# Optimization experiments

Measured on AMD Instinct MI355X. Metric: run time of the kernel, lower is better.

The kernel has to match this reference:

```python
import jax, jax.numpy as jnp
import numpy as np

B = 16384      # batch (rollout size)
OBS = 64       # obs_dim
ACT = 8        # action_dim
H = 128        # hidden_dim
NN = 4         # num_neighbors
N = NN + 1     # num_nodes in local graph
HEADS = 2
SLOPE = 0.2    # leaky_relu negative slope


def setup_inputs() -> dict:
    key = jax.random.key(0)
    ks = jax.random.split(key, 20)

    def glorot(k, shape):
        fan_in, fan_out = shape[0], shape[-1]
        lim = np.sqrt(6.0 / (fan_in + fan_out)).astype(np.float32)
        return jax.random.uniform(k, shape, jnp.float32, -lim, lim)

    obs = jax.random.normal(ks[0], (B, OBS), jnp.float32)
    neighbor_obs = jax.random.normal(ks[1], (B, NN, OBS), jnp.float32)
    adj = jax.random.randint(ks[2], (B, N), 0, 2, jnp.int32)
    adj = adj.at[:, 0].set(1)  # self node always connected (avoids all -inf rows)

    params = dict(
        enc_w1=glorot(ks[3], (OBS, H)), enc_b1=jnp.zeros((H,), jnp.float32),
        enc_w2=glorot(ks[4], (H, H)),  enc_b2=jnp.zeros((H,), jnp.float32),
        gat_w=glorot(ks[5], (HEADS, H, H)),       # per-head W (no bias)
        gat_a=glorot(ks[6], (HEADS, 2 * H)),      # per-head attention vector a
        val_w1=glorot(ks[7], (H * HEADS, H)), val_b1=jnp.zeros((H,), jnp.float32),
        val_w2=glorot(ks[8], (H, 1)),          val_b2=jnp.zeros((1,), jnp.float32),
        pol_w1=glorot(ks[9], (H * HEADS, H)), pol_b1=jnp.zeros((H,), jnp.float32),
        pol_w2=glorot(ks[10], (H, ACT)),       pol_b2=jnp.zeros((ACT,), jnp.float32),
    )
    return {"obs": obs, "neighbor_obs": neighbor_obs, "adj": adj, **params}


def reference(obs, neighbor_obs, adj,
              enc_w1, enc_b1, enc_w2, enc_b2,
              gat_w, gat_a,
              val_w1, val_b1, val_w2, val_b2,
              pol_w1, pol_b1, pol_w2, pol_b2):
    # shared local encoder applied to self obs and each neighbor obs
    all_obs = jnp.concatenate([obs[:, None, :], neighbor_obs], axis=1)   # [B,N,OBS]
    emb = jax.nn.relu(all_obs @ enc_w1 + enc_b1) @ enc_w2 + enc_b2       # [B,N,H]

    # GAT layer (all heads vectorized). Concat attention a^T[Wh_i||Wh_j]
    # decomposes into a1.Wh_i + a2.Wh_j.
    Wh = jnp.einsum('bnd,hdo->bhno', emb, gat_w)                          # [B,heads,N,H]
    a1, a2 = gat_a[:, :H], gat_a[:, H:]
    ei = jnp.einsum('bhno,ho->bhn', Wh, a1)                               # [B,heads,N]
    ej = jnp.einsum('bhno,ho->bhn', Wh, a2)
    e = jax.nn.leaky_relu(ei[..., :, None] + ej[..., None, :], SLOPE)     # [B,heads,N,N]
    # torch masked_fill broadcasts adj [B,N] as a column mask over j
    e = jnp.where((adj == 0)[:, None, None, :], -jnp.inf, e)
    attn = jax.nn.softmax(e, axis=-1)                                     # [B,heads,N,N]
    h_prime = jnp.einsum('bhij,bhjo->bhio', attn, Wh)                     # [B,heads,N,H]

    # node 0 (the agent itself), heads concatenated (head-major order, as torch cat)
    final = h_prime[:, :, 0, :].reshape(h_prime.shape[0], HEADS * H)      # [B,heads*H]

    value = jax.nn.relu(final @ val_w1 + val_b1) @ val_w2 + val_b2        # [B,1]
    logits = jax.nn.relu(final @ pol_w1 + pol_b1) @ pol_w2 + pol_b2      # [B,ACT]
    return value, logits
```

## Files before the change

kernel.cpp:

```cpp
#include <hip/hip_runtime.h>
#include <hip/hip_bf16.h>

#define B_TOT 16384

typedef __attribute__((ext_vector_type(8))) short short8;
typedef __attribute__((ext_vector_type(4))) short short4v;
typedef __attribute__((ext_vector_type(4))) float f32x4;

__device__ __forceinline__ float bf2f(short s){
  unsigned u = ((unsigned)(unsigned short)s) << 16;
  return __uint_as_float(u);
}
__device__ __forceinline__ short f2bf(float f){
  __hip_bfloat16 h = __float2bfloat16(f);
  return *reinterpret_cast<short*>(&h);
}

#define MFMA16(a,b,c) __builtin_amdgcn_mfma_f32_16x16x32_bf16(a,b,c,0,0,0)

#define W_W1T   0
#define W_W2T   8192
#define W_GWT   24576
#define W_HW1T  57344
#define W_PW2T  122880
#define W_VW2   123904
#define W_NELEM 124032
#define CVEC_BYTE 248064
#define MIX_BYTE  250112
#define PREP_TOT  124544

__global__ void prep_weights(const float* __restrict__ enc_w1, const float* __restrict__ enc_w2,
                             const float* __restrict__ gat_w, const float* __restrict__ gat_a,
                             const float* __restrict__ val_w1, const float* __restrict__ pol_w1,
                             const float* __restrict__ pol_w2, const float* __restrict__ val_w2,
                             unsigned short* __restrict__ wt, float* __restrict__ cvec){
  int t = blockIdx.x*256 + threadIdx.x;
  if (t < W_NELEM){
    float v;
    if (t < 8192){ int c=t>>6, k=t&63; v = enc_w1[k*128 + c]; }
    else if (t < 24576){ int u=t-8192, c=u>>7, k=u&127; v = enc_w2[k*128 + c]; }
    else if (t < 57344){ int u=t-24576, h=u>>14, r=u&16383, c=r>>7, k=r&127; v = gat_w[h*16384 + k*128 + c]; }
    else if (t < 122880){ int u=t-57344, oc=u>>8, k=u&255; v = (oc<128) ? val_w1[k*128+oc] : pol_w1[k*128+(oc-128)]; }
    else if (t < 123904){ int u=t-122880, a=u>>7, k=u&127; v = pol_w2[k*8+a]; }
    else { int u=t-123904; v = val_w2[u]; }
    wt[t] = (unsigned short)(unsigned)*reinterpret_cast<unsigned short*>(&(__hip_bfloat16&)(*(__hip_bfloat16*)&v));
  } else if (t < PREP_TOT){
    int q = t - W_NELEM;
    int vsel = q >> 7, d = q & 127;
    int h = vsel >> 1, s2 = vsel & 1;
    const float* gw = gat_w + h*16384 + d*128;
    const float* aa = gat_a + h*256 + s2*128;
    float s = 0.f;
    for (int o=0;o<128;++o) s += gw[o]*aa[o];
    cvec[vsel*128 + d] = s;
  }
}

__global__ void prep_weights2(const float* __restrict__ enc_w1, const float* __restrict__ enc_w2,
                              const float* __restrict__ gat_w, const float* __restrict__ gat_a,
                              const float* __restrict__ val_w1, const float* __restrict__ pol_w1,
                              const float* __restrict__ pol_w2, const float* __restrict__ val_w2,
                              unsigned short* __restrict__ wt, float* __restrict__ cvec){
  int t = blockIdx.x*256 + threadIdx.x;
  if (t < W_NELEM){
    float v;
    if (t < 8192){ int c=t>>6, k=t&63; v = enc_w1[k*128 + c]; }
    else if (t < 24576){ int u=t-8192, c=u>>7, k=u&127; v = enc_w2[k*128 + c]; }
    else if (t < 57344){ int u=t-24576, h=u>>14, r=u&16383, c=r>>7, k=r&127; v = gat_w[h*16384 + k*128 + c]; }
    else if (t < 122880){ int u=t-57344, oc=u>>8, k=u&255; v = (oc<128) ? val_w1[k*128+oc] : pol_w1[k*128+(oc-128)]; }
    else if (t < 123904){ int u=t-122880, a=u>>7, k=u&127; v = pol_w2[k*8+a]; }
    else { int u=t-123904; v = val_w2[u]; }
    short b = f2bf(v);
    wt[t] = (unsigned short)b;
  } else if (t < PREP_TOT){
    int q = t - W_NELEM;
    int vsel = q >> 7, d = q & 127;
    int h = vsel >> 1, s2 = vsel & 1;
    const float* gw = gat_w + h*16384 + d*128;
    const float* aa = gat_a + h*256 + s2*128;
    float s = 0.f;
    for (int o=0;o<128;++o) s += gw[o]*aa[o];
    cvec[vsel*128 + d] = s;
  }
}

#define K1_LDS 30720

__global__ __launch_bounds__(256, 2) void enc_gat(
    const float* __restrict__ obs, const float* __restrict__ nobs, const int* __restrict__ adjp,
    const float* __restrict__ enc_b1, const float* __restrict__ enc_b2,
    const unsigned short* __restrict__ wt_all, const float* __restrict__ cvec,
    unsigned short* __restrict__ mixws)
{
  __shared__ __align__(16) char lds[K1_LDS];
  const int tid  = threadIdx.x;
  const int lane = tid & 63;
  const int wv   = tid >> 6;
  const int lm   = lane & 15;
  const int grp  = lane >> 4;
  const int kb   = grp * 8;
  const int gblk = blockIdx.x * 16;

  const unsigned short* w1t = wt_all + W_W1T;
  const unsigned short* w2t = wt_all + W_W2T;

  #pragma unroll
  for (int i = 0; i < 5; ++i){
    int chunk = i*256 + tid;
    int row = chunk >> 4;
    int c4  = (chunk & 15) * 4;
    int a = row/5, n = row%5;
    const float* src = n ? (nobs + ((size_t)(gblk+a)*4 + (n-1))*64 + c4)
                         : (obs  + (size_t)(gblk+a)*64 + c4);
    float4 v = *reinterpret_cast<const float4*>(src);
    short4v p = { f2bf(v.x), f2bf(v.y), f2bf(v.z), f2bf(v.w) };
    *reinterpret_cast<short4v*>(lds + ((row*128 + c4*2) ^ ((row & 7) << 4))) = p;
  }
  __syncthreads();

  const int c0 = wv*32 + lm, c1 = c0 + 16;

  f32x4 acc[5][2];
  #pragma unroll
  for (int mt=0; mt<5; ++mt){ acc[mt][0]=(f32x4){0,0,0,0}; acc[mt][1]=(f32x4){0,0,0,0}; }
  #pragma unroll
  for (int ks=0; ks<2; ++ks){
    short8 b0 = *reinterpret_cast<const short8*>(w1t + c0*64 + ks*32 + kb);
    short8 b1 = *reinterpret_cast<const short8*>(w1t + c1*64 + ks*32 + kb);
    #pragma unroll
    for (int mt=0; mt<5; ++mt){
      int row = mt*16 + lm;
      short8 a = *reinterpret_cast<short8*>(lds + ((row*128 + (ks*32+kb)*2) ^ ((row&7)<<4)));
      acc[mt][0] = MFMA16(a, b0, acc[mt][0]);
      acc[mt][1] = MFMA16(a, b1, acc[mt][1]);
    }
  }
  {
    float bv0 = enc_b1[c0], bv1 = enc_b1[c1];
    #pragma unroll
    for (int mt=0; mt<5; ++mt)
      #pragma unroll
      for (int j=0; j<4; ++j){
        int row = mt*16 + grp*4 + j;
        *reinterpret_cast<short*>(lds + 10240 + ((row*256 + c0*2) ^ ((row&7)<<4)))
            = f2bf(fmaxf(acc[mt][0][j] + bv0, 0.f));
        *reinterpret_cast<short*>(lds + 10240 + ((row*256 + c1*2) ^ ((row&7)<<4)))
            = f2bf(fmaxf(acc[mt][1][j] + bv1, 0.f));
      }
  }
  __syncthreads();

  f32x4 acc2[5][2];
  #pragma unroll
  for (int mt=0; mt<5; ++mt){ acc2[mt][0]=(f32x4){0,0,0,0}; acc2[mt][1]=(f32x4){0,0,0,0}; }
  #pragma unroll
  for (int ks=0; ks<4; ++ks){
    short8 b0 = *reinterpret_cast<const short8*>(w2t + c0*128 + ks*32 + kb);
    short8 b1 = *reinterpret_cast<const short8*>(w2t + c1*128 + ks*32 + kb);
    #pragma unroll
    for (int mt=0; mt<5; ++mt){
      int row = mt*16 + lm;
      short8 a = *reinterpret_cast<short8*>(lds + 10240 + ((row*256 + (ks*32+kb)*2) ^ ((row&7)<<4)));
      acc2[mt][0] = MFMA16(a, b0, acc2[mt][0]);
      acc2[mt][1] = MFMA16(a, b1, acc2[mt][1]);
    }
  }
  __syncthreads();
  {
    float b20 = enc_b2[c0], b21 = enc_b2[c1];
    #pragma unroll
    for (int mt=0; mt<5; ++mt)
      #pragma unroll
      for (int j=0; j<4; ++j){
        int row = mt*16 + grp*4 + j;
        *reinterpret_cast<short*>(lds + ((row*256 + c0*2) ^ ((row&7)<<4)))
            = f2bf(acc2[mt][0][j] + b20);
        *reinterpret_cast<short*>(lds + ((row*256 + c1*2) ^ ((row&7)<<4)))
            = f2bf(acc2[mt][1][j] + b21);
      }
  }
  __syncthreads();

  const int ag = wv*4 + grp;
  const int ga = gblk + ag;
  float ef[5][8];
  #pragma unroll
  for (int n=0; n<5; ++n){
    int row = ag*5 + n;
    short8 er = *reinterpret_cast<short8*>(lds + ((row*256 + lm*16) ^ ((row&7)<<4)));
    #pragma unroll
    for (int e=0; e<8; ++e) ef[n][e] = bf2f(er[e]);
  }
  int msk[5];
  #pragma unroll
  for (int n=0; n<5; ++n) msk[n] = adjp[(size_t)ga*5 + n];

  #pragma unroll
  for (int h=0; h<2; ++h){
    float c1v[8], c2v[8];
    #pragma unroll
    for (int e=0; e<8; ++e){
      c1v[e] = cvec[(2*h  )*128 + lm*8 + e];
      c2v[e] = cvec[(2*h+1)*128 + lm*8 + e];
    }
    float ei = 0.f;
    #pragma unroll
    for (int e=0; e<8; ++e) ei += ef[0][e]*c1v[e];
    ei += __shfl_xor(ei,1); ei += __shfl_xor(ei,2); ei += __shfl_xor(ei,4); ei += __shfl_xor(ei,8);

    float at[5]; float mx = -1e30f;
    #pragma unroll
    for (int n=0; n<5; ++n){
      float t = 0.f;
      #pragma unroll
      for (int e=0; e<8; ++e) t += ef[n][e]*c2v[e];
      t += __shfl_xor(t,1); t += __shfl_xor(t,2); t += __shfl_xor(t,4); t += __shfl_xor(t,8);
      float s = ei + t;
      s = (s > 0.f) ? s : 0.2f*s;
      at[n] = s;
      if (msk[n] && s > mx) mx = s;
    }
    float den = 0.f;
    #pragma unroll
    for (int n=0; n<5; ++n){
      float e2 = msk[n] ? __expf(at[n]-mx) : 0.f;
      at[n] = e2; den += e2;
    }
    float inv = 1.f/den;
    short8 o;
    #pragma unroll
    for (int e=0; e<8; ++e){
      float s = 0.f;
      #pragma unroll
      for (int n=0; n<5; ++n) s += at[n]*ef[n][e];
      o[e] = f2bf(s*inv);
    }
    *reinterpret_cast<short8*>(mixws + (size_t)ga*256 + h*128 + lm*8) = o;
  }
}

#define T_LDS 32768

__global__ __launch_bounds__(256, 2) void tail_k(
    const unsigned short* __restrict__ mixws, const unsigned short* __restrict__ wt_all,
    const float* __restrict__ val_b1, const float* __restrict__ val_b2,
    const float* __restrict__ pol_b1, const float* __restrict__ pol_b2,
    float* __restrict__ dout)
{
  __shared__ __align__(16) char lds[T_LDS];
  const int tid  = threadIdx.x;
  const int lane = tid & 63;
  const int wv   = tid >> 6;
  const int lm   = lane & 15;
  const int grp  = lane >> 4;
  const int kb   = grp * 8;
  const int gb   = blockIdx.x * 32;

  const unsigned short* gwt  = wt_all + W_GWT;
  const unsigned short* hw1t = wt_all + W_HW1T;
  const unsigned short* pw2t = wt_all + W_PW2T;
  const unsigned short* vw2  = wt_all + W_VW2;

  #pragma unroll
  for (int i=0; i<4; ++i){
    int chunk = i*256 + tid;
    int row = chunk >> 5;
    int c8  = (chunk & 31) * 8;
    short8 v = *reinterpret_cast<const short8*>(mixws + (size_t)(gb+row)*256 + c8);
    *reinterpret_cast<short8*>(lds + ((row*512 + c8*2) ^ ((row&7)<<4))) = v;
  }
  __syncthreads();

  const int hh = wv >> 1, half = wv & 1;
  f32x4 fac[2][4];
  #pragma unroll
  for (int mt=0; mt<2; ++mt)
    #pragma unroll
    for (int nt=0; nt<4; ++nt) fac[mt][nt] = (f32x4){0,0,0,0};
  #pragma unroll
  for (int ks=0; ks<4; ++ks){
    short8 a0 = *reinterpret_cast<short8*>(lds + (((lm   )*512 + (hh*128+ks*32+kb)*2) ^ ((lm&7)<<4)));
    short8 a1 = *reinterpret_cast<short8*>(lds + (((16+lm)*512 + (hh*128+ks*32+kb)*2) ^ ((lm&7)<<4)));
    #pragma unroll
    for (int nt=0; nt<4; ++nt){
      short8 b = *reinterpret_cast<const short8*>(gwt + hh*16384 + (half*64+nt*16+lm)*128 + ks*32 + kb);
      fac[0][nt] = MFMA16(a0, b, fac[0][nt]);
      fac[1][nt] = MFMA16(a1, b, fac[1][nt]);
    }
  }
  #pragma unroll
  for (int mt=0; mt<2; ++mt)
    #pragma unroll
    for (int nt=0; nt<4; ++nt)
      #pragma unroll
      for (int j=0; j<4; ++j){
        int row = mt*16 + grp*4 + j;
        int col = hh*128 + half*64 + nt*16 + lm;
        *reinterpret_cast<short*>(lds + 16384 + ((row*512 + col*2) ^ ((row&7)<<4)))
            = f2bf(fac[mt][nt][j]);
      }
  __syncthreads();

  f32x4 hac[2][4];
  #pragma unroll
  for (int mt=0; mt<2; ++mt)
    #pragma unroll
    for (int nt=0; nt<4; ++nt) hac[mt][nt] = (f32x4){0,0,0,0};
  #pragma unroll
  for (int ks=0; ks<8; ++ks){
    short8 a0 = *reinterpret_cast<short8*>(lds + 16384 + (((lm   )*512 + (ks*32+kb)*2) ^ ((lm&7)<<4)));
    short8 a1 = *reinterpret_cast<short8*>(lds + 16384 + (((16+lm)*512 + (ks*32+kb)*2) ^ ((lm&7)<<4)));
    #pragma unroll
    for (int nt=0; nt<4; ++nt){
      short8 b = *reinterpret_cast<const short8*>(hw1t + (wv*64+nt*16+lm)*256 + ks*32 + kb);
      hac[0][nt] = MFMA16(a0, b, hac[0][nt]);
      hac[1][nt] = MFMA16(a1, b, hac[1][nt]);
    }
  }
  #pragma unroll
  for (int nt=0; nt<4; ++nt){
    int oc = wv*64 + nt*16 + lm;
    float bv = (oc < 128) ? val_b1[oc] : pol_b1[oc-128];
    #pragma unroll
    for (int mt=0; mt<2; ++mt)
      #pragma unroll
      for (int j=0; j<4; ++j){
        int row = mt*16 + grp*4 + j;
        *reinterpret_cast<short*>(lds + ((row*512 + oc*2) ^ ((row&7)<<4)))
            = f2bf(fmaxf(hac[mt][nt][j] + bv, 0.f));
      }
  }
  __syncthreads();

  {
    int a = tid >> 3, act = tid & 7;
    float s = pol_b2[act];
    #pragma unroll
    for (int i=0; i<16; ++i){
      short8 v = *reinterpret_cast<short8*>(lds + ((a*512 + (128 + i*8)*2) ^ ((a&7)<<4)));
      short8 w = *reinterpret_cast<const short8*>(pw2t + act*128 + i*8);
      #pragma unroll
      for (int e=0; e<8; ++e) s += bf2f(v[e]) * bf2f(w[e]);
    }
    dout[B_TOT + (size_t)(gb + a)*8 + act] = s;
  }
  if (tid < 64){
    int a = tid >> 1, hf = tid & 1;
    float s = 0.f;
    #pragma unroll
    for (int i=0; i<8; ++i){
      short8 v = *reinterpret_cast<short8*>(lds + ((a*512 + (hf*64 + i*8)*2) ^ ((a&7)<<4)));
      short8 w = *reinterpret_cast<const short8*>(vw2 + hf*64 + i*8);
      #pragma unroll
      for (int e=0; e<8; ++e) s += bf2f(v[e]) * bf2f(w[e]);
    }
    s += __shfl_xor(s, 1);
    if (!hf) dout[gb + a] = s + val_b2[0];
  }
}

extern "C" void kernel_launch(void* const* d_in, const int* in_sizes, int n_in,
                              void* d_out, int out_size, void* d_ws, size_t ws_size,
                              hipStream_t stream) {
  (void)in_sizes; (void)n_in; (void)out_size; (void)ws_size;
  const float* obs    = (const float*)d_in[0];
  const float* nobs   = (const float*)d_in[1];
  const int*   adj    = (const int*)  d_in[2];
  const float* enc_w1 = (const float*)d_in[3];
  const float* enc_b1 = (const float*)d_in[4];
  const float* enc_w2 = (const float*)d_in[5];
  const float* enc_b2 = (const float*)d_in[6];
  const float* gat_w  = (const float*)d_in[7];
  const float* gat_a  = (const float*)d_in[8];
  const float* val_w1 = (const float*)d_in[9];
  const float* val_b1 = (const float*)d_in[10];
  const float* val_w2 = (const float*)d_in[11];
  const float* val_b2 = (const float*)d_in[12];
  const float* pol_w1 = (const float*)d_in[13];
  const float* pol_b1 = (const float*)d_in[14];
  const float* pol_w2 = (const float*)d_in[15];
  const float* pol_b2 = (const float*)d_in[16];

  unsigned short* wt    = (unsigned short*)d_ws;
  float*          cvec  = (float*)((char*)d_ws + CVEC_BYTE);
  unsigned short* mixws = (unsigned short*)((char*)d_ws + MIX_BYTE);

  prep_weights2<<<(PREP_TOT + 255)/256, 256, 0, stream>>>(
      enc_w1, enc_w2, gat_w, gat_a, val_w1, pol_w1, pol_w2, val_w2, wt, cvec);

  enc_gat<<<B_TOT/16, 256, 0, stream>>>(
      obs, nobs, adj, enc_b1, enc_b2, wt, cvec, mixws);

  tail_k<<<B_TOT/32, 256, 0, stream>>>(
      mixws, wt, val_b1, val_b2, pol_b1, pol_b2, (float*)d_out);
}
```

Baseline: 131.9 us.

## Fuse encoder/GAT and head kernels into one kernel with interleaved weight layout

Merges the encoder+GAT kernel and the tail MLP kernel into a single kernel per 16-agent block, keeping the mixed GAT output in LDS instead of writing it to and reading it back from a global workspace. Weights are repacked in prep so each lane's even/odd output columns are adjacent, which allows packed 32-bit bf16 stores to LDS instead of scalar 16-bit stores. Launch bounds are raised to four blocks per CU. The tail now works on 16 rows per block instead of 32, so weight reuse per block halves and the extra-occupancy bound may force register pressure.

```diff
diff --git a/kernel.cpp b/kernel.cpp
--- a/kernel.cpp
+++ b/kernel.cpp
@@ -10,6 +10,10 @@
 __device__ __forceinline__ float bf2f(short s){
   unsigned u = ((unsigned)(unsigned short)s) << 16;
   return __uint_as_float(u);
+}
+__device__ __forceinline__ unsigned f2bfu(float f){
+  __hip_bfloat16 h = __float2bfloat16(f);
+  return (unsigned)*reinterpret_cast<unsigned short*>(&h);
 }
 __device__ __forceinline__ short f2bf(float f){
   __hip_bfloat16 h = __float2bfloat16(f);
@@ -26,7 +30,6 @@
 #define W_VW2   123904
 #define W_NELEM 124032
 #define CVEC_BYTE 248064
-#define MIX_BYTE  250112
 #define PREP_TOT  124544
 
 __global__ void prep_weights(const float* __restrict__ enc_w1, const float* __restrict__ enc_w2,
@@ -35,64 +38,65 @@
                              const float* __restrict__ pol_w2, const float* __restrict__ val_w2,
                              unsigned short* __restrict__ wt, float* __restrict__ cvec){
   int t = blockIdx.x*256 + threadIdx.x;
+  if (t >= PREP_TOT) return;
   if (t < W_NELEM){
-    float v;
-    if (t < 8192){ int c=t>>6, k=t&63; v = enc_w1[k*128 + c]; }
-    else if (t < 24576){ int u=t-8192, c=u>>7, k=u&127; v = enc_w2[k*128 + c]; }
-    else if (t < 57344){ int u=t-24576, h=u>>14, r=u&16383, c=r>>7, k=r&127; v = gat_w[h*16384 + k*128 + c]; }
-    else if (t < 122880){ int u=t-57344, oc=u>>8, k=u&255; v = (oc<128) ? val_w1[k*128+oc] : pol_w1[k*128+(oc-128)]; }
-    else if (t < 123904){ int u=t-122880, a=u>>7, k=u&127; v = pol_w2[k*8+a]; }
-    else { int u=t-123904; v = val_w2[u]; }
-    wt[t] = (unsigned short)(unsigned)*reinterpret_cast<unsigned short*>(&(__hip_bfloat16&)(*(__hip_bfloat16*)&v));
-  } else if (t < PREP_TOT){
+    float v; int idx;
+    if (t < 8192){
+      int c = t >> 6, k = t & 63;
+      int G = c >> 5, r = c & 31, b = r & 1, f = r >> 1;
+      idx = ((G*2 + b)*16 + f)*64 + k;
+      v = enc_w1[k*128 + c];
+    } else if (t < 24576){
+      int u = t - 8192, c = u >> 7, k = u & 127;
+      int G = c >> 5, r = c & 31, b = r & 1, f = r >> 1;
+      idx = 8192 + ((G*2 + b)*16 + f)*128 + k;
+      v = enc_w2[k*128 + c];
+    } else if (t < 57344){
+      int u = t - 24576, h = u >> 14, r2 = u & 16383, o = r2 >> 7, d = r2 & 127;
+      int G = o >> 5, r = o & 31, b = r & 1, f = r >> 1;
+      idx = 24576 + h*16384 + ((G*2 + b)*16 + f)*128 + d;
+      v = gat_w[h*16384 + d*128 + o];
+    } else if (t < 122880){
+      int u = t - 57344, oc = u >> 8, k = u & 255;
+      int G = oc >> 5, r = oc & 31, b = r & 1, f = r >> 1;
+      idx = 57344 + ((G*2 + b)*16 + f)*256 + k;
+      v = (oc < 128) ? val_w1[k*128 + oc] : pol_w1[k*128 + (oc - 128)];
+    } else if (t < 123904){
+      int u = t - 122880, a = u >> 7, k = u & 127;
+      idx = t;
+      v = pol_w2[k*8 + a];
+    } else {
+      idx = t;
+      v = val_w2[t - 123904];
+    }
+    wt[idx] = (unsigned short)f2bfu(v);
+  } else {
     int q = t - W_NELEM;
     int vsel = q >> 7, d = q & 127;
     int h = vsel >> 1, s2 = vsel & 1;
     const float* gw = gat_w + h*16384 + d*128;
     const float* aa = gat_a + h*256 + s2*128;
     float s = 0.f;
-    for (int o=0;o<128;++o) s += gw[o]*aa[o];
+    #pragma unroll 4
+    for (int o = 0; o < 128; ++o) s += gw[o]*aa[o];
     cvec[vsel*128 + d] = s;
   }
 }
 
-__global__ void prep_weights2(const float* __restrict__ enc_w1, const float* __restrict__ enc_w2,
-                              const float* __restrict__ gat_w, const float* __restrict__ gat_a,
-                              const float* __restrict__ val_w1, const float* __restrict__ pol_w1,
-                              const float* __restrict__ pol_w2, const float* __restrict__ val_w2,
-                              unsigned short* __restrict__ wt, float* __restrict__ cvec){
-  int t = blockIdx.x*256 + threadIdx.x;
-  if (t < W_NELEM){
-    float v;
-    if (t < 8192){ int c=t>>6, k=t&63; v = enc_w1[k*128 + c]; }
-    else if (t < 24576){ int u=t-8192, c=u>>7, k=u&127; v = enc_w2[k*128 + c]; }
-    else if (t < 57344){ int u=t-24576, h=u>>14, r=u&16383, c=r>>7, k=r&127; v = gat_w[h*16384 + k*128 + c]; }
-    else if (t < 122880){ int u=t-57344, oc=u>>8, k=u&255; v = (oc<128) ? val_w1[k*128+oc] : pol_w1[k*128+(oc-128)]; }
-    else if (t < 123904){ int u=t-122880, a=u>>7, k=u&127; v = pol_w2[k*8+a]; }
-    else { int u=t-123904; v = val_w2[u]; }
-    short b = f2bf(v);
-    wt[t] = (unsigned short)b;
-  } else if (t < PREP_TOT){
-    int q = t - W_NELEM;
-    int vsel = q >> 7, d = q & 127;
-    int h = vsel >> 1, s2 = vsel & 1;
-    const float* gw = gat_w + h*16384 + d*128;
-    const float* aa = gat_a + h*256 + s2*128;
-    float s = 0.f;
-    for (int o=0;o<128;++o) s += gw[o]*aa[o];
-    cvec[vsel*128 + d] = s;
-  }
-}
-
-#define K1_LDS 30720
-
-__global__ __launch_bounds__(256, 2) void enc_gat(
+#define MIX_L   20480
+#define FINAL_L 0
+#define H2_L    8192
+#define K_LDS   30720
+
+__global__ __launch_bounds__(256, 4) void colight_fused(
     const float* __restrict__ obs, const float* __restrict__ nobs, const int* __restrict__ adjp,
     const float* __restrict__ enc_b1, const float* __restrict__ enc_b2,
+    const float* __restrict__ val_b1, const float* __restrict__ val_b2,
+    const float* __restrict__ pol_b1, const float* __restrict__ pol_b2,
     const unsigned short* __restrict__ wt_all, const float* __restrict__ cvec,
-    unsigned short* __restrict__ mixws)
+    float* __restrict__ dout)
 {
-  __shared__ __align__(16) char lds[K1_LDS];
+  __shared__ __align__(16) char lds[K_LDS];
   const int tid  = threadIdx.x;
   const int lane = tid & 63;
   const int wv   = tid >> 6;
@@ -101,8 +105,12 @@
   const int kb   = grp * 8;
   const int gblk = blockIdx.x * 16;
 
-  const unsigned short* w1t = wt_all + W_W1T;
-  const unsigned short* w2t = wt_all + W_W2T;
+  const unsigned short* w1t  = wt_all + W_W1T;
+  const unsigned short* w2t  = wt_all + W_W2T;
+  const unsigned short* gwt  = wt_all + W_GWT;
+  const unsigned short* hw1t = wt_all + W_HW1T;
+  const unsigned short* pw2t = wt_all + W_PW2T;
+  const unsigned short* vw2  = wt_all + W_VW2;
 
   #pragma unroll
   for (int i = 0; i < 5; ++i){
@@ -118,244 +126,211 @@
   }
   __syncthreads();
 
-  const int c0 = wv*32 + lm, c1 = c0 + 16;
-
-  f32x4 acc[5][2];
-  #pragma unroll
-  for (int mt=0; mt<5; ++mt){ acc[mt][0]=(f32x4){0,0,0,0}; acc[mt][1]=(f32x4){0,0,0,0}; }
-  #pragma unroll
-  for (int ks=0; ks<2; ++ks){
-    short8 b0 = *reinterpret_cast<const short8*>(w1t + c0*64 + ks*32 + kb);
-    short8 b1 = *reinterpret_cast<const short8*>(w1t + c1*64 + ks*32 + kb);
-    #pragma unroll
-    for (int mt=0; mt<5; ++mt){
-      int row = mt*16 + lm;
-      short8 a = *reinterpret_cast<short8*>(lds + ((row*128 + (ks*32+kb)*2) ^ ((row&7)<<4)));
-      acc[mt][0] = MFMA16(a, b0, acc[mt][0]);
-      acc[mt][1] = MFMA16(a, b1, acc[mt][1]);
-    }
-  }
-  {
-    float bv0 = enc_b1[c0], bv1 = enc_b1[c1];
+  {
+    f32x4 aE[5], aO[5];
+    #pragma unroll
+    for (int mt=0; mt<5; ++mt){ aE[mt]=(f32x4){0,0,0,0}; aO[mt]=(f32x4){0,0,0,0}; }
+    #pragma unroll
+    for (int ks=0; ks<2; ++ks){
+      short8 bE = *reinterpret_cast<const short8*>(w1t + ((wv*2+0)*16 + lm)*64 + ks*32 + kb);
+      short8 bO = *reinterpret_cast<const short8*>(w1t + ((wv*2+1)*16 + lm)*64 + ks*32 + kb);
+      #pragma unroll
+      for (int mt=0; mt<5; ++mt){
+        int row = mt*16 + lm;
+        short8 a = *reinterpret_cast<short8*>(lds + ((row*128 + (ks*32+kb)*2) ^ ((row&7)<<4)));
+        aE[mt] = MFMA16(a, bE, aE[mt]);
+        aO[mt] = MFMA16(a, bO, aO[mt]);
+      }
+    }
+    const int ce = 32*wv + 2*lm;
+    const float be = enc_b1[ce], bo = enc_b1[ce+1];
     #pragma unroll
     for (int mt=0; mt<5; ++mt)
       #pragma unroll
       for (int j=0; j<4; ++j){
         int row = mt*16 + grp*4 + j;
-        *reinterpret_cast<short*>(lds + 10240 + ((row*256 + c0*2) ^ ((row&7)<<4)))
-            = f2bf(fmaxf(acc[mt][0][j] + bv0, 0.f));
-        *reinterpret_cast<short*>(lds + 10240 + ((row*256 + c1*2) ^ ((row&7)<<4)))
-            = f2bf(fmaxf(acc[mt][1][j] + bv1, 0.f));
-      }
-  }
-  __syncthreads();
-
-  f32x4 acc2[5][2];
-  #pragma unroll
-  for (int mt=0; mt<5; ++mt){ acc2[mt][0]=(f32x4){0,0,0,0}; acc2[mt][1]=(f32x4){0,0,0,0}; }
-  #pragma unroll
-  for (int ks=0; ks<4; ++ks){
-    short8 b0 = *reinterpret_cast<const short8*>(w2t + c0*128 + ks*32 + kb);
-    short8 b1 = *reinterpret_cast<const short8*>(w2t + c1*128 + ks*32 + kb);
-    #pragma unroll
-    for (int mt=0; mt<5; ++mt){
-      int row = mt*16 + lm;
-      short8 a = *reinterpret_cast<short8*>(lds + 10240 + ((row*256 + (ks*32+kb)*2) ^ ((row&7)<<4)));
-      acc2[mt][0] = MFMA16(a, b0, acc2[mt][0]);
-      acc2[mt][1] = MFMA16(a, b1, acc2[mt][1]);
-    }
-  }
-  __syncthreads();
-  {
-    float b20 = enc_b2[c0], b21 = enc_b2[c1];
+        unsigned pk = f2bfu(fmaxf(aE[mt][j] + be, 0.f))
+                    | (f2bfu(fmaxf(aO[mt][j] + bo, 0.f)) << 16);
+        *reinterpret_cast<unsigned*>(lds + 10240 + ((row*256 + ce*2) ^ ((row&7)<<4))) = pk;
+      }
+  }
+  __syncthreads();
+
+  {
+    f32x4 aE[5], aO[5];
+    #pragma unroll
+    for (int mt=0; mt<5; ++mt){ aE[mt]=(f32x4){0,0,0,0}; aO[mt]=(f32x4){0,0,0,0}; }
+    #pragma unroll
+    for (int ks=0; ks<4; ++ks){
+      short8 bE = *reinterpret_cast<const short8*>(w2t + ((wv*2+0)*16 + lm)*128 + ks*32 + kb);
+      short8 bO = *reinterpret_cast<const short8*>(w2t + ((wv*2+1)*16 + lm)*128 + ks*32 + kb);
+      #pragma unroll
+      for (int mt=0; mt<5; ++mt){
+        int row = mt*16 + lm;
+        short8 a = *reinterpret_cast<short8*>(lds + 10240 + ((row*256 + (ks*32+kb)*2) ^ ((row&7)<<4)));
+        aE[mt] = MFMA16(a, bE, aE[mt]);
+        aO[mt] = MFMA16(a, bO, aO[mt]);
+      }
+    }
+    __syncthreads();
+    const int ce = 32*wv + 2*lm;
+    const float be = enc_b2[ce], bo = enc_b2[ce+1];
     #pragma unroll
     for (int mt=0; mt<5; ++mt)
       #pragma unroll
       for (int j=0; j<4; ++j){
         int row = mt*16 + grp*4 + j;
-        *reinterpret_cast<short*>(lds + ((row*256 + c0*2) ^ ((row&7)<<4)))
-            = f2bf(acc2[mt][0][j] + b20);
-        *reinterpret_cast<short*>(lds + ((row*256 + c1*2) ^ ((row&7)<<4)))
-            = f2bf(acc2[mt][1][j] + b21);
-      }
-  }
-  __syncthreads();
-
-  const int ag = wv*4 + grp;
-  const int ga = gblk + ag;
-  float ef[5][8];
-  #pragma unroll
-  for (int n=0; n<5; ++n){
-    int row = ag*5 + n;
-    short8 er = *reinterpret_cast<short8*>(lds + ((row*256 + lm*16) ^ ((row&7)<<4)));
-    #pragma unroll
-    for (int e=0; e<8; ++e) ef[n][e] = bf2f(er[e]);
-  }
-  int msk[5];
-  #pragma unroll
-  for (int n=0; n<5; ++n) msk[n] = adjp[(size_t)ga*5 + n];
-
-  #pragma unroll
-  for (int h=0; h<2; ++h){
-    float c1v[8], c2v[8];
-    #pragma unroll
-    for (int e=0; e<8; ++e){
-      c1v[e] = cvec[(2*h  )*128 + lm*8 + e];
-      c2v[e] = cvec[(2*h+1)*128 + lm*8 + e];
-    }
-    float ei = 0.f;
-    #pragma unroll
-    for (int e=0; e<8; ++e) ei += ef[0][e]*c1v[e];
-    ei += __shfl_xor(ei,1); ei += __shfl_xor(ei,2); ei += __shfl_xor(ei,4); ei += __shfl_xor(ei,8);
-
-    float at[5]; float mx = -1e30f;
+        unsigned pk = f2bfu(aE[mt][j] + be) | (f2bfu(aO[mt][j] + bo) << 16);
+        *reinterpret_cast<unsigned*>(lds + ((row*256 + ce*2) ^ ((row&7)<<4))) = pk;
+      }
+  }
+  __syncthreads();
+
+  {
+    const int ag = wv*4 + grp;
+    const int ga = gblk + ag;
+    float ef[5][8];
     #pragma unroll
     for (int n=0; n<5; ++n){
-      float t = 0.f;
-      #pragma unroll
-      for (int e=0; e<8; ++e) t += ef[n][e]*c2v[e];
-      t += __shfl_xor(t,1); t += __shfl_xor(t,2); t += __shfl_xor(t,4); t += __shfl_xor(t,8);
-      float s = ei + t;
-      s = (s > 0.f) ? s : 0.2f*s;
-      at[n] = s;
-      if (msk[n] && s > mx) mx = s;
-    }
-    float den = 0.f;
-    #pragma unroll
-    for (int n=0; n<5; ++n){
-      float e2 = msk[n] ? __expf(at[n]-mx) : 0.f;
-      at[n] = e2; den += e2;
-    }
-    float inv = 1.f/den;
-    short8 o;
-    #pragma unroll
-    for (int e=0; e<8; ++e){
-      float s = 0.f;
-      #pragma unroll
-      for (int n=0; n<5; ++n) s += at[n]*ef[n][e];
-      o[e] = f2bf(s*inv);
-    }
-    *reinterpret_cast<short8*>(mixws + (size_t)ga*256 + h*128 + lm*8) = o;
-  }
-}
-
-#define T_LDS 32768
-
-__global__ __launch_bounds__(256, 2) void tail_k(
-    const unsigned short* __restrict__ mixws, const unsigned short* __restrict__ wt_all,
-    const float* __restrict__ val_b1, const float* __restrict__ val_b2,
-    const float* __restrict__ pol_b1, const float* __restrict__ pol_b2,
-    float* __restrict__ dout)
-{
-  __shared__ __align__(16) char lds[T_LDS];
-  const int tid  = threadIdx.x;
-  const int lane = tid & 63;
-  const int wv   = tid >> 6;
-  const int lm   = lane & 15;
-  const int grp  = lane >> 4;
-  const int kb   = grp * 8;
-  const int gb   = blockIdx.x * 32;
-
-  const unsigned short* gwt  = wt_all + W_GWT;
-  const unsigned short* hw1t = wt_all + W_HW1T;
-  const unsigned short* pw2t = wt_all + W_PW2T;
-  const unsigned short* vw2  = wt_all + W_VW2;
-
-  #pragma unroll
-  for (int i=0; i<4; ++i){
-    int chunk = i*256 + tid;
-    int row = chunk >> 5;
-    int c8  = (chunk & 31) * 8;
-    short8 v = *reinterpret_cast<const short8*>(mixws + (size_t)(gb+row)*256 + c8);
-    *reinterpret_cast<short8*>(lds + ((row*512 + c8*2) ^ ((row&7)<<4))) = v;
-  }
-  __syncthreads();
-
-  const int hh = wv >> 1, half = wv & 1;
-  f32x4 fac[2][4];
-  #pragma unroll
-  for (int mt=0; mt<2; ++mt)
-    #pragma unroll
-    for (int nt=0; nt<4; ++nt) fac[mt][nt] = (f32x4){0,0,0,0};
-  #pragma unroll
-  for (int ks=0; ks<4; ++ks){
-    short8 a0 = *reinterpret_cast<short8*>(lds + (((lm   )*512 + (hh*128+ks*32+kb)*2) ^ ((lm&7)<<4)));
-    short8 a1 = *reinterpret_cast<short8*>(lds + (((16+lm)*512 + (hh*128+ks*32+kb)*2) ^ ((lm&7)<<4)));
-    #pragma unroll
-    for (int nt=0; nt<4; ++nt){
-      short8 b = *reinterpret_cast<const short8*>(gwt + hh*16384 + (half*64+nt*16+lm)*128 + ks*32 + kb);
-      fac[0][nt] = MFMA16(a0, b, fac[0][nt]);
-      fac[1][nt] = MFMA16(a1, b, fac[1][nt]);
-    }
-  }
-  #pragma unroll
-  for (int mt=0; mt<2; ++mt)
-    #pragma unroll
-    for (int nt=0; nt<4; ++nt)
+      int row = ag*5 + n;
+      short8 er = *reinterpret_cast<short8*>(lds + ((row*256 + lm*16) ^ ((row&7)<<4)));
+      #pragma unroll
+      for (int e=0; e<8; ++e) ef[n][e] = bf2f(er[e]);
+    }
+    int msk[5];
+    #pragma unroll
+    for (int n=0; n<5; ++n) msk[n] = adjp[(size_t)ga*5 + n];
+
+    #pragma unroll
+    for (int h=0; h<2; ++h){
+      float c1v[8], c2v[8];
+      #pragma unroll
+      for (int e=0; e<8; ++e){
+        c1v[e] = cvec[(2*h  )*128 + lm*8 + e];
+        c2v[e] = cvec[(2*h+1)*128 + lm*8 + e];
+      }
+      float ei = 0.f;
+      #pragma unroll
+      for (int e=0; e<8; ++e) ei += ef[0][e]*c1v[e];
+      ei += __shfl_xor(ei,1); ei += __shfl_xor(ei,2); ei += __shfl_xor(ei,4); ei += __shfl_xor(ei,8);
+
+      float at[5]; float mx = -1e30f;
+      #pragma unroll
+      for (int n=0; n<5; ++n){
+        float t = 0.f;
+        #pragma unroll
+        for (int e=0; e<8; ++e) t += ef[n][e]*c2v[e];
+        t += __shfl_xor(t,1); t += __shfl_xor(t,2); t += __shfl_xor(t,4); t += __shfl_xor(t,8);
+        float s = ei + t;
+        s = (s > 0.f) ? s : 0.2f*s;
+        at[n] = s;
+        if (msk[n] && s > mx) mx = s;
+      }
+      float den = 0.f;
+      #pragma unroll
+      for (int n=0; n<5; ++n){
+        float e2 = msk[n] ? __expf(at[n]-mx) : 0.f;
+        at[n] = e2; den += e2;
+      }
+      float inv = 1.f/den;
+      short8 o;
+      #pragma unroll
+      for (int e=0; e<8; ++e){
+        float s = 0.f;
+        #pragma unroll
+        for (int n=0; n<5; ++n) s += at[n]*ef[n][e];
+        o[e] = f2bf(s*inv);
+      }
+      *reinterpret_cast<short8*>(lds + MIX_L + ((ag*512 + (h*128 + lm*8)*2) ^ ((ag&7)<<4))) = o;
+    }
+  }
+  __syncthreads();
+
+  {
+    const int hh = wv >> 1, half = wv & 1;
+    f32x4 fE[2], fO[2];
+    #pragma unroll
+    for (int g2=0; g2<2; ++g2){ fE[g2]=(f32x4){0,0,0,0}; fO[g2]=(f32x4){0,0,0,0}; }
+    #pragma unroll
+    for (int ks=0; ks<4; ++ks){
+      short8 a = *reinterpret_cast<short8*>(lds + MIX_L + ((lm*512 + (hh*128 + ks*32 + kb)*2) ^ ((lm&7)<<4)));
+      #pragma unroll
+      for (int g2=0; g2<2; ++g2){
+        int G = half*2 + g2;
+        short8 bE = *reinterpret_cast<const short8*>(gwt + hh*16384 + ((G*2+0)*16 + lm)*128 + ks*32 + kb);
+        short8 bO = *reinterpret_cast<const short8*>(gwt + hh*16384 + ((G*2+1)*16 + lm)*128 + ks*32 + kb);
+        fE[g2] = MFMA16(a, bE, fE[g2]);
+        fO[g2] = MFMA16(a, bO, fO[g2]);
+      }
+    }
+    #pragma unroll
+    for (int g2=0; g2<2; ++g2){
+      int cb = hh*128 + half*64 + 32*g2 + 2*lm;
       #pragma unroll
       for (int j=0; j<4; ++j){
-        int row = mt*16 + grp*4 + j;
-        int col = hh*128 + half*64 + nt*16 + lm;
-        *reinterpret_cast<short*>(lds + 16384 + ((row*512 + col*2) ^ ((row&7)<<4)))
-            = f2bf(fac[mt][nt][j]);
-      }
-  __syncthreads();
-
-  f32x4 hac[2][4];
-  #pragma unroll
-  for (int mt=0; mt<2; ++mt)
-    #pragma unroll
-    for (int nt=0; nt<4; ++nt) hac[mt][nt] = (f32x4){0,0,0,0};
-  #pragma unroll
-  for (int ks=0; ks<8; ++ks){
-    short8 a0 = *reinterpret_cast<short8*>(lds + 16384 + (((lm   )*512 + (ks*32+kb)*2) ^ ((lm&7)<<4)));
-    short8 a1 = *reinterpret_cast<short8*>(lds + 16384 + (((16+lm)*512 + (ks*32+kb)*2) ^ ((lm&7)<<4)));
-    #pragma unroll
-    for (int nt=0; nt<4; ++nt){
-      short8 b = *reinterpret_cast<const short8*>(hw1t + (wv*64+nt*16+lm)*256 + ks*32 + kb);
-      hac[0][nt] = MFMA16(a0, b, hac[0][nt]);
-      hac[1][nt] = MFMA16(a1, b, hac[1][nt]);
-    }
-  }
-  #pragma unroll
-  for (int nt=0; nt<4; ++nt){
-    int oc = wv*64 + nt*16 + lm;
-    float bv = (oc < 128) ? val_b1[oc] : pol_b1[oc-128];
-    #pragma unroll
-    for (int mt=0; mt<2; ++mt)
+        int row = grp*4 + j;
+        unsigned pk = f2bfu(fE[g2][j]) | (f2bfu(fO[g2][j]) << 16);
+        *reinterpret_cast<unsigned*>(lds + FINAL_L + ((row*512 + cb*2) ^ ((row&7)<<4))) = pk;
+      }
+    }
+  }
+  __syncthreads();
+
+  {
+    f32x4 hE[2], hO[2];
+    #pragma unroll
+    for (int g2=0; g2<2; ++g2){ hE[g2]=(f32x4){0,0,0,0}; hO[g2]=(f32x4){0,0,0,0}; }
+    #pragma unroll
+    for (int ks=0; ks<8; ++ks){
+      short8 a = *reinterpret_cast<short8*>(lds + FINAL_L + ((lm*512 + (ks*32+kb)*2) ^ ((lm&7)<<4)));
+      #pragma unroll
+      for (int g2=0; g2<2; ++g2){
+        int G = 2*wv + g2;
+        short8 bE = *reinterpret_cast<const short8*>(hw1t + ((G*2+0)*16 + lm)*256 + ks*32 + kb);
+        short8 bO = *reinterpret_cast<const short8*>(hw1t + ((G*2+1)*16 + lm)*256 + ks*32 + kb);
+        hE[g2] = MFMA16(a, bE, hE[g2]);
+        hO[g2] = MFMA16(a, bO, hO[g2]);
+      }
+    }
+    #pragma unroll
+    for (int g2=0; g2<2; ++g2){
+      int oc = 64*wv + 32*g2 + 2*lm;
+      float be = (oc   < 128) ? val_b1[oc]   : pol_b1[oc-128];
+      float bo = (oc+1 < 128) ? val_b1[oc+1] : pol_b1[oc-127];
       #pragma unroll
       for (int j=0; j<4; ++j){
-        int row = mt*16 + grp*4 + j;
-        *reinterpret_cast<short*>(lds + ((row*512 + oc*2) ^ ((row&7)<<4)))
-            = f2bf(fmaxf(hac[mt][nt][j] + bv, 0.f));
-      }
-  }
-  __syncthreads();
-
-  {
+        int row = grp*4 + j;
+        unsigned pk = f2bfu(fmaxf(hE[g2][j] + be, 0.f))
+                    | (f2bfu(fmaxf(hO[g2][j] + bo, 0.f)) << 16);
+        *reinterpret_cast<unsigned*>(lds + H2_L + ((row*512 + oc*2) ^ ((row&7)<<4))) = pk;
+      }
+    }
+  }
+  __syncthreads();
+
+  if (tid < 128){
     int a = tid >> 3, act = tid & 7;
     float s = pol_b2[act];
     #pragma unroll
     for (int i=0; i<16; ++i){
-      short8 v = *reinterpret_cast<short8*>(lds + ((a*512 + (128 + i*8)*2) ^ ((a&7)<<4)));
+      short8 v = *reinterpret_cast<short8*>(lds + H2_L + ((a*512 + (128 + i*8)*2) ^ ((a&7)<<4)));
       short8 w = *reinterpret_cast<const short8*>(pw2t + act*128 + i*8);
       #pragma unroll
       for (int e=0; e<8; ++e) s += bf2f(v[e]) * bf2f(w[e]);
     }
-    dout[B_TOT + (size_t)(gb + a)*8 + act] = s;
-  }
-  if (tid < 64){
-    int a = tid >> 1, hf = tid & 1;
+    dout[B_TOT + (size_t)(gblk + a)*8 + act] = s;
+  } else if (tid < 160){
+    int q = tid - 128, a = q >> 1, hf = q & 1;
     float s = 0.f;
     #pragma unroll
     for (int i=0; i<8; ++i){
-      short8 v = *reinterpret_cast<short8*>(lds + ((a*512 + (hf*64 + i*8)*2) ^ ((a&7)<<4)));
+      short8 v = *reinterpret_cast<short8*>(lds + H2_L + ((a*512 + (hf*64 + i*8)*2) ^ ((a&7)<<4)));
       short8 w = *reinterpret_cast<const short8*>(vw2 + hf*64 + i*8);
       #pragma unroll
       for (int e=0; e<8; ++e) s += bf2f(v[e]) * bf2f(w[e]);
     }
     s += __shfl_xor(s, 1);
-    if (!hf) dout[gb + a] = s + val_b2[0];
+    if (!hf) dout[gblk + a] = s + val_b2[0];
   }
 }
 
@@ -381,16 +356,14 @@
   const float* pol_w2 = (const float*)d_in[15];
   const float* pol_b2 = (const float*)d_in[16];
 
-  unsigned short* wt    = (unsigned short*)d_ws;
-  float*          cvec  = (float*)((char*)d_ws + CVEC_BYTE);
-  unsigned short* mixws = (unsigned short*)((char*)d_ws + MIX_BYTE);
-
-  prep_weights2<<<(PREP_TOT + 255)/256, 256, 0, stream>>>(
+  unsigned short* wt   = (unsigned short*)d_ws;
+  float*          cvec = (float*)((char*)d_ws + CVEC_BYTE);
+
+  prep_weights<<<(PREP_TOT + 255)/256, 256, 0, stream>>>(
       enc_w1, enc_w2, gat_w, gat_a, val_w1, pol_w1, pol_w2, val_w2, wt, cvec);
 
-  enc_gat<<<B_TOT/16, 256, 0, stream>>>(
-      obs, nobs, adj, enc_b1, enc_b2, wt, cvec, mixws);
-
-  tail_k<<<B_TOT/32, 256, 0, stream>>>(
-      mixws, wt, val_b1, val_b2, pol_b1, pol_b2, (float*)d_out);
-}
+  colight_fused<<<B_TOT/16, 256, 0, stream>>>(
+      obs, nobs, adj, enc_b1, enc_b2,
+      val_b1, val_b2, pol_b1, pol_b2,
+      wt, cvec, (float*)d_out);
+}
```

Result: slower. 136.5 us (+3.5%).
